# Kernel optimization log

Hardware: AMD Instinct MI355X
Metric: run time of the kernel (lower is better)

Reference implementation:

```python
import jax, jax.numpy as jnp
import numpy as np

B, N, F, C = 8, 4096, 1024, 64


def setup_inputs() -> dict:
    key = jax.random.key(0)
    k1, k2, k3 = jax.random.split(key, 3)
    x1 = jax.random.normal(k1, (B, N, F), dtype=jnp.float32)
    x2 = jax.random.normal(k2, (B, N, F), dtype=jnp.float32)
    W = jax.random.normal(k3, (C, F), dtype=jnp.float32) / np.sqrt(F)
    b = jnp.zeros((C,), dtype=jnp.float32)
    return {"x1": x1, "x2": x2, "W": W, "b": b}


def _select_max(x, W, b):
    # x: [B, N, F] -> scores [B, N, C]
    scores = jnp.einsum("bnf,cf->bnc", x, W) + b
    # per-batch, per-class index of max-scoring instance: [B, C]
    idx = jnp.argmax(scores, axis=1)
    # gather the selected instance feature vectors: [B, C, F]
    return jnp.take_along_axis(x, idx[:, :, None], axis=1)


def reference(x1, x2, W, b):
    d = _select_max(x1, W, b)
    d1 = _select_max(x2, W, b)
    return (d, d1)
```

## Files before the change

### kernel.cpp

```cpp
#include <hip/hip_runtime.h>

#define B_   8
#define N_   4096
#define F_   1024
#define C_   64
#define NBLK 16
#define MARGIN 0.08f

typedef __attribute__((ext_vector_type(8))) short bhalf8;
typedef __attribute__((ext_vector_type(4))) float f32x4;
typedef __attribute__((ext_vector_type(4))) unsigned short us4;

__device__ __forceinline__ unsigned short f2bf_rne(float x) {
    unsigned u = __builtin_bit_cast(unsigned, x);
    u += 0x7fffu + ((u >> 16) & 1u);
    return (unsigned short)(u >> 16);
}
__device__ __forceinline__ bhalf8 cvt8(float4 a, float4 b) {
    bhalf8 r;
    r[0] = (short)f2bf_rne(a.x); r[1] = (short)f2bf_rne(a.y);
    r[2] = (short)f2bf_rne(a.z); r[3] = (short)f2bf_rne(a.w);
    r[4] = (short)f2bf_rne(b.x); r[5] = (short)f2bf_rne(b.y);
    r[6] = (short)f2bf_rne(b.z); r[7] = (short)f2bf_rne(b.w);
    return r;
}

#define LEXGT(a, ai, b, bi) ((a) > (b) || ((a) == (b) && (ai) < (bi)))
#define INSERT3(vv, nn)                                                        \
    do {                                                                       \
        float _v = (vv); int _n = (nn);                                        \
        if (LEXGT(_v, _n, v0, i0)) { v2=v1; i2=i1; v1=v0; i1=i0; v0=_v; i0=_n; } \
        else if (LEXGT(_v, _n, v1, i1)) { v2=v1; i2=i1; v1=_v; i1=_n; }        \
        else if (LEXGT(_v, _n, v2, i2)) { v2=_v; i2=_n; }                      \
    } while (0)
#define INSERT4(vv, nn)                                                        \
    do {                                                                       \
        float _v = (vv); int _n = (nn);                                        \
        if (LEXGT(_v, _n, v0, i0)) { v3=v2; i3=i2; v2=v1; i2=i1; v1=v0; i1=i0; v0=_v; i0=_n; } \
        else if (LEXGT(_v, _n, v1, i1)) { v3=v2; i3=i2; v2=v1; i2=i1; v1=_v; i1=_n; } \
        else if (LEXGT(_v, _n, v2, i2)) { v3=v2; i3=i2; v2=_v; i2=_n; }        \
        else if (LEXGT(_v, _n, v3, i3)) { v3=_v; i3=_n; }                      \
    } while (0)

__global__ __launch_bounds__(256) void wconv_kernel(
    const float* __restrict__ W, unsigned short* __restrict__ Wh)
{
    int i = blockIdx.x * 256 + threadIdx.x;
    float4 v = ((const float4*)W)[i];
    us4 hh;
    hh[0] = f2bf_rne(v.x); hh[1] = f2bf_rne(v.y);
    hh[2] = f2bf_rne(v.z); hh[3] = f2bf_rne(v.w);
    ((us4*)Wh)[i] = hh;
}

__global__ __launch_bounds__(1024, 4) void score_top_kernel(
    const float* __restrict__ x1, const float* __restrict__ x2,
    const unsigned short* __restrict__ Wh,
    float* __restrict__ pv, int* __restrict__ pi)
{
    __shared__ __align__(16) char lds[131072];

    const int tid  = threadIdx.x;
    const int nb   = blockIdx.x;
    const int b    = blockIdx.y;
    const int inp  = blockIdx.z;
    const float* __restrict__ x = inp ? x2 : x1;

    const int lane = tid & 63;
    const int w    = tid >> 6;
    const int rsel = lane & 15;
    const int g    = lane >> 4;
    const int swz  = (rsel & 7) << 4;

    const int row = nb * 256 + w * 16 + rsel;
    const float* __restrict__ xr = x + ((size_t)b * N_ + row) * F_ + g * 8;

    f32x4 acc[4];
    #pragma unroll
    for (int nt = 0; nt < 4; ++nt) acc[nt] = (f32x4){0.f, 0.f, 0.f, 0.f};

#define LOADX(dst, kc)                                                         \
    do {                                                                       \
        _Pragma("unroll")                                                      \
        for (int st = 0; st < 4; ++st) {                                       \
            dst[2 * st]     = *(const float4*)(xr + (kc) * 128 + st * 32);     \
            dst[2 * st + 1] = *(const float4*)(xr + (kc) * 128 + st * 32 + 4); \
        }                                                                      \
        __builtin_amdgcn_sched_barrier(0);                                     \
    } while (0)

#define COMPUTE(src, kc)                                                       \
    do {                                                                       \
        _Pragma("unroll")                                                      \
        for (int st = 0; st < 4; ++st) {                                       \
            bhalf8 ah = cvt8(src[2 * st], src[2 * st + 1]);                    \
            int kb = (kc) * 256 + st * 64 + g * 16;                            \
            _Pragma("unroll")                                                  \
            for (int nt = 0; nt < 4; ++nt) {                                   \
                int cls = nt * 16 + rsel;                                      \
                bhalf8 bf = *(const bhalf8*)(lds + ((cls * 2048 + kb) ^ swz)); \
                acc[nt] = __builtin_amdgcn_mfma_f32_16x16x32_bf16(ah, bf, acc[nt], 0, 0, 0); \
            }                                                                  \
        }                                                                      \
        __builtin_amdgcn_sched_barrier(0);                                     \
    } while (0)

    float4 xa[8], xb[8];
    LOADX(xa, 0);

    #pragma unroll
    for (int j = 0; j < 8; ++j) {
        int gi = tid + 1024 * j;
        int c = gi >> 7, kq = gi & 127;
        bhalf8 v = *(const bhalf8*)(Wh + (size_t)c * F_ + kq * 8);
        *(bhalf8*)(lds + ((c * 2048 + kq * 16) ^ ((c & 7) << 4))) = v;
    }
    __syncthreads();

    #pragma unroll
    for (int kc = 0; kc < 8; kc += 2) {
        LOADX(xb, kc + 1);
        COMPUTE(xa, kc);
        if (kc + 2 < 8) LOADX(xa, kc + 2);
        COMPUTE(xb, kc + 1);
    }

    float wv0[4], wv1[4], wv2[4]; int wi0[4], wi1[4], wi2[4];
    #pragma unroll
    for (int nt = 0; nt < 4; ++nt) {
        float v0 = -3.4e38f, v1 = -3.4e38f, v2 = -3.4e38f;
        int   i0 = 0x7fffffff, i1 = 0x7fffffff, i2 = 0x7fffffff;
        #pragma unroll
        for (int r = 0; r < 4; ++r) {
            int n = nb * 256 + w * 16 + 4 * g + r;
            INSERT3(acc[nt][r], n);
        }
        #pragma unroll
        for (int d = 16; d <= 32; d <<= 1) {
            float u0 = __shfl_xor(v0, d), u1 = __shfl_xor(v1, d), u2 = __shfl_xor(v2, d);
            int   j0 = __shfl_xor(i0, d), j1 = __shfl_xor(i1, d), j2 = __shfl_xor(i2, d);
            INSERT3(u0, j0); INSERT3(u1, j1); INSERT3(u2, j2);
        }
        wv0[nt] = v0; wv1[nt] = v1; wv2[nt] = v2;
        wi0[nt] = i0; wi1[nt] = i1; wi2[nt] = i2;
    }

    __syncthreads();
    float* tv = (float*)lds;
    int*   ti = (int*)(lds + 16384);
    if (lane < 16) {
        #pragma unroll
        for (int nt = 0; nt < 4; ++nt) {
            int c = nt * 16 + lane;
            tv[(w * C_ + c) * 3 + 0] = wv0[nt]; ti[(w * C_ + c) * 3 + 0] = wi0[nt];
            tv[(w * C_ + c) * 3 + 1] = wv1[nt]; ti[(w * C_ + c) * 3 + 1] = wi1[nt];
            tv[(w * C_ + c) * 3 + 2] = wv2[nt]; ti[(w * C_ + c) * 3 + 2] = wi2[nt];
        }
    }
    __syncthreads();

    if (tid < C_) {
        int c = tid;
        float v0 = -3.4e38f, v1 = -3.4e38f, v2 = -3.4e38f, v3 = -3.4e38f;
        int   i0 = 0x7fffffff, i1 = 0x7fffffff, i2 = 0x7fffffff, i3 = 0x7fffffff;
        #pragma unroll 4
        for (int ww = 0; ww < 16; ++ww)
            #pragma unroll
            for (int k = 0; k < 3; ++k)
                INSERT4(tv[(ww * C_ + c) * 3 + k], ti[(ww * C_ + c) * 3 + k]);
        int blk = ((inp * B_ + b) * NBLK + nb);
        pv[(blk * C_ + c) * 4 + 0] = v0; pi[(blk * C_ + c) * 4 + 0] = i0;
        pv[(blk * C_ + c) * 4 + 1] = v1; pi[(blk * C_ + c) * 4 + 1] = i1;
        pv[(blk * C_ + c) * 4 + 2] = v2; pi[(blk * C_ + c) * 4 + 2] = i2;
        pv[(blk * C_ + c) * 4 + 3] = v3; pi[(blk * C_ + c) * 4 + 3] = i3;
    }
}

__global__ __launch_bounds__(64) void select_gather_kernel(
    const float* __restrict__ x1, const float* __restrict__ x2,
    const float* __restrict__ W,
    const float* __restrict__ pv, const int* __restrict__ pi,
    float* __restrict__ out)
{
    const int c   = blockIdx.x;
    const int b   = blockIdx.y;
    const int inp = blockIdx.z;
    const int tid = threadIdx.x;

    const int nb = tid >> 2, k = tid & 3;
    const int blk = ((inp * B_ + b) * NBLK + nb);
    const int myoff = (blk * C_ + c) * 4 + k;
    float v  = pv[myoff];
    int   id = pi[myoff];

    float m = v;
    #pragma unroll
    for (int d = 32; d; d >>= 1) m = fmaxf(m, __shfl_xor(m, d));

    unsigned long long mask = __ballot(v >= m - MARGIN);
    const float* __restrict__ x = inp ? x2 : x1;

    int winner;
    if (__popcll(mask) == 1) {
        winner = __shfl(id, __ffsll(mask) - 1);
    } else {
        float bv = -3.4e38f; int bn = 0x7fffffff;
        unsigned long long mm = mask;
        while (mm) {
            int l = __ffsll(mm) - 1; mm &= mm - 1;
            int n = __shfl(id, l);
            const float4* xrow = (const float4*)(x + ((size_t)b * N_ + n) * F_) + tid * 4;
            const float4* wrow = (const float4*)(W + (size_t)c * F_) + tid * 4;
            float p = 0.f;
            #pragma unroll
            for (int q = 0; q < 4; ++q) {
                float4 xv = xrow[q], wq = wrow[q];
                p += xv.x * wq.x + xv.y * wq.y + xv.z * wq.z + xv.w * wq.w;
            }
            #pragma unroll
            for (int d = 32; d; d >>= 1) p += __shfl_xor(p, d);
            if (p > bv || (p == bv && n < bn)) { bv = p; bn = n; }
        }
        winner = bn;
    }

    const float4* src = (const float4*)(x + ((size_t)b * N_ + winner) * F_);
    float4* dst = (float4*)(out + (((size_t)inp * B_ + b) * C_ + c) * F_);
    #pragma unroll
    for (int q = 0; q < 4; ++q) dst[tid + 64 * q] = src[tid + 64 * q];
}

extern "C" void kernel_launch(void* const* d_in, const int* in_sizes, int n_in,
                              void* d_out, int out_size, void* d_ws, size_t ws_size,
                              hipStream_t stream) {
    const float* x1 = (const float*)d_in[0];
    const float* x2 = (const float*)d_in[1];
    const float* W  = (const float*)d_in[2];

    unsigned short* Wh = (unsigned short*)d_ws;
    float* pv = (float*)((char*)d_ws + (size_t)C_ * F_ * sizeof(unsigned short));
    int*   pi = (int*)((char*)pv + (size_t)2 * B_ * NBLK * C_ * 4 * sizeof(float));

    wconv_kernel<<<C_ * F_ / 1024, 256, 0, stream>>>(W, Wh);
    dim3 g1(NBLK, B_, 2);
    score_top_kernel<<<g1, 1024, 0, stream>>>(x1, x2, Wh, pv, pi);
    dim3 g2(C_, B_, 2);
    select_gather_kernel<<<g2, 64, 0, stream>>>(x1, x2, W, pv, pi, (float*)d_out);
}
```

Baseline: 72.94 us.

## Use inline-asm global loads with explicit vmcnt waits for double-buffered x streaming

Replaces compiler-scheduled float4 loads of x with inline-assembly global_load_dwordx4 batches and explicit s_waitcnt vmcnt(8) waits. This keeps the next chunk's loads in flight while the current chunk is computed on MFMA, so the compiler cannot insert conservative waits. It also caps the candidate list in the select kernel at 8 entries and hoists the W row pointer, which can drop candidates if more than 8 fall within the margin. The hand-written asm relies on exact vmcnt accounting and fixed offsets.

```diff
diff --git a/kernel.cpp b/kernel.cpp
--- a/kernel.cpp
+++ b/kernel.cpp
@@ -79,13 +79,27 @@
     #pragma unroll
     for (int nt = 0; nt < 4; ++nt) acc[nt] = (f32x4){0.f, 0.f, 0.f, 0.f};
 
-#define LOADX(dst, kc)                                                         \
-    do {                                                                       \
-        _Pragma("unroll")                                                      \
-        for (int st = 0; st < 4; ++st) {                                       \
-            dst[2 * st]     = *(const float4*)(xr + (kc) * 128 + st * 32);     \
-            dst[2 * st + 1] = *(const float4*)(xr + (kc) * 128 + st * 32 + 4); \
-        }                                                                      \
+#define ISSUE(buf, t)                                                          \
+    do {                                                                       \
+        const float* a_ = xr + (t) * 128;                                      \
+        asm volatile(                                                          \
+            "global_load_dwordx4 %0, %8, off\n\t"                              \
+            "global_load_dwordx4 %1, %8, off offset:16\n\t"                    \
+            "global_load_dwordx4 %2, %8, off offset:128\n\t"                   \
+            "global_load_dwordx4 %3, %8, off offset:144\n\t"                   \
+            "global_load_dwordx4 %4, %8, off offset:256\n\t"                   \
+            "global_load_dwordx4 %5, %8, off offset:272\n\t"                   \
+            "global_load_dwordx4 %6, %8, off offset:384\n\t"                   \
+            "global_load_dwordx4 %7, %8, off offset:400"                       \
+            : "=v"(buf[0]), "=v"(buf[1]), "=v"(buf[2]), "=v"(buf[3]),          \
+              "=v"(buf[4]), "=v"(buf[5]), "=v"(buf[6]), "=v"(buf[7])           \
+            : "v"(a_));                                                        \
+        __builtin_amdgcn_sched_barrier(0);                                     \
+    } while (0)
+
+#define WAITV(n)                                                               \
+    do {                                                                       \
+        asm volatile("s_waitcnt vmcnt(" #n ")" ::: "memory");                  \
         __builtin_amdgcn_sched_barrier(0);                                     \
     } while (0)
 
@@ -102,11 +116,10 @@
                 acc[nt] = __builtin_amdgcn_mfma_f32_16x16x32_bf16(ah, bf, acc[nt], 0, 0, 0); \
             }                                                                  \
         }                                                                      \
-        __builtin_amdgcn_sched_barrier(0);                                     \
     } while (0)
 
     float4 xa[8], xb[8];
-    LOADX(xa, 0);
+    ISSUE(xa, 0);
 
     #pragma unroll
     for (int j = 0; j < 8; ++j) {
@@ -117,13 +130,15 @@
     }
     __syncthreads();
 
-    #pragma unroll
-    for (int kc = 0; kc < 8; kc += 2) {
-        LOADX(xb, kc + 1);
-        COMPUTE(xa, kc);
-        if (kc + 2 < 8) LOADX(xa, kc + 2);
-        COMPUTE(xb, kc + 1);
-    }
+    ISSUE(xb, 1);
+    WAITV(8);  COMPUTE(xa, 0);  ISSUE(xa, 2);
+    WAITV(8);  COMPUTE(xb, 1);  ISSUE(xb, 3);
+    WAITV(8);  COMPUTE(xa, 2);  ISSUE(xa, 4);
+    WAITV(8);  COMPUTE(xb, 3);  ISSUE(xb, 5);
+    WAITV(8);  COMPUTE(xa, 4);  ISSUE(xa, 6);
+    WAITV(8);  COMPUTE(xb, 5);  ISSUE(xb, 7);
+    WAITV(8);  COMPUTE(xa, 6);
+    WAITV(0);  COMPUTE(xb, 7);
 
     float wv0[4], wv1[4], wv2[4]; int wi0[4], wi1[4], wi2[4];
     #pragma unroll
@@ -182,35 +197,40 @@
     const float* __restrict__ pv, const int* __restrict__ pi,
     float* __restrict__ out)
 {
-    const int c   = blockIdx.x;
-    const int b   = blockIdx.y;
-    const int inp = blockIdx.z;
-    const int tid = threadIdx.x;
-
-    const int nb = tid >> 2, k = tid & 3;
-    const int blk = ((inp * B_ + b) * NBLK + nb);
-    const int myoff = (blk * C_ + c) * 4 + k;
-    float v  = pv[myoff];
-    int   id = pi[myoff];
+    const int c    = blockIdx.x;
+    const int b    = blockIdx.y;
+    const int inp  = blockIdx.z;
+    const int lane = threadIdx.x;
+
+    const int nbk = lane >> 2, k = lane & 3;
+    const int blk = ((inp * B_ + b) * NBLK + nbk);
+    const int off = (blk * C_ + c) * 4 + k;
+    const float v = pv[off];
+    const int  id = pi[off];
 
     float m = v;
     #pragma unroll
     for (int d = 32; d; d >>= 1) m = fmaxf(m, __shfl_xor(m, d));
-
-    unsigned long long mask = __ballot(v >= m - MARGIN);
+    const float thr = m - MARGIN;
+
+    unsigned long long mask = __ballot(v >= thr);
+    int cand[8]; int nc = 0;
+    while (mask) {
+        int l = __ffsll(mask) - 1; mask &= mask - 1;
+        int n = __shfl(id, l);
+        if (nc < 8) cand[nc++] = n;
+    }
+
     const float* __restrict__ x = inp ? x2 : x1;
-
     int winner;
-    if (__popcll(mask) == 1) {
-        winner = __shfl(id, __ffsll(mask) - 1);
+    if (nc == 1) {
+        winner = cand[0];
     } else {
         float bv = -3.4e38f; int bn = 0x7fffffff;
-        unsigned long long mm = mask;
-        while (mm) {
-            int l = __ffsll(mm) - 1; mm &= mm - 1;
-            int n = __shfl(id, l);
-            const float4* xrow = (const float4*)(x + ((size_t)b * N_ + n) * F_) + tid * 4;
-            const float4* wrow = (const float4*)(W + (size_t)c * F_) + tid * 4;
+        const float4* wrow = (const float4*)(W + (size_t)c * F_) + lane * 4;
+        for (int kk = 0; kk < nc; ++kk) {
+            int n = cand[kk];
+            const float4* xrow = (const float4*)(x + ((size_t)b * N_ + n) * F_) + lane * 4;
             float p = 0.f;
             #pragma unroll
             for (int q = 0; q < 4; ++q) {
@@ -227,7 +247,7 @@
     const float4* src = (const float4*)(x + ((size_t)b * N_ + winner) * F_);
     float4* dst = (float4*)(out + (((size_t)inp * B_ + b) * C_ + c) * F_);
     #pragma unroll
-    for (int q = 0; q < 4; ++q) dst[tid + 64 * q] = src[tid + 64 * q];
+    for (int q = 0; q < 4; ++q) dst[lane + 64 * q] = src[lane + 64 * q];
 }
 
 extern "C" void kernel_launch(void* const* d_in, const int* in_sizes, int n_in,
```

Result: no change. 73.23 us (+0.4%).
